# Performance work log

Hardware: AMD Instinct MI355X
Metric: run time of the kernel (lower is better)

Reference implementation:

```python
import jax, jax.numpy as jnp
import numpy as np

GRID_SIZE = 5
SPLINE_ORDER = 3


def _haar_filters():
    # db1 (Haar) decomposition filters, matching wavelet.create_wavelet_filter:
    # dec_lo[::-1] = [s, s], dec_hi[::-1] = [s, -s]; rec filters are identical for Haar.
    s = np.float32(1.0 / np.sqrt(2.0))
    lo = np.array([s, s], np.float32)
    hi = np.array([s, -s], np.float32)
    # f = a.unsqueeze(0) * b.unsqueeze(1)  ->  f[p, q] = a[q] * b[p]
    def outer(a, b):
        return b[:, None] * a[None, :]
    dec = np.stack([outer(lo, lo), outer(lo, hi), outer(hi, lo), outer(hi, hi)], 0)  # (4,2,2): LL,LH,HL,HH
    return jnp.asarray(dec), jnp.asarray(dec)


def depthwise_conv5(x, w, b):
    # torch Conv2d(C, C, 5, padding='same', groups=C)
    y = jax.lax.conv_general_dilated(
        x, w, window_strides=(1, 1), padding=[(2, 2), (2, 2)],
        dimension_numbers=('NCHW', 'OIHW', 'NCHW'), feature_group_count=x.shape[1])
    return y + b[None, :, None, None]


def kan_linear(x, base_w, spline_w, scaler):
    # efficient-kan KANLinear: base SiLU linear + B-spline linear over last dim.
    in_f = x.shape[-1]
    out_f = base_w.shape[0]
    shp = x.shape
    xf = x.reshape(-1, in_f)                      # (N, in)
    h = 2.0 / GRID_SIZE                           # grid_range [-1, 1]
    grid_1d = jnp.arange(-SPLINE_ORDER, GRID_SIZE + SPLINE_ORDER + 1, dtype=xf.dtype) * h - 1.0
    grid = jnp.broadcast_to(grid_1d, (in_f, grid_1d.shape[0]))  # (in, G+2k+1)
    xe = xf[:, :, None]
    bases = ((xe >= grid[:, :-1]) & (xe < grid[:, 1:])).astype(xf.dtype)
    for k in range(1, SPLINE_ORDER + 1):
        bases = ((xe - grid[:, :-(k + 1)]) / (grid[:, k:-1] - grid[:, :-(k + 1)]) * bases[..., :-1]
                 + (grid[:, k + 1:] - xe) / (grid[:, k + 1:] - grid[:, 1:-k]) * bases[..., 1:])
    # bases: (N, in, G+k)
    base_out = jax.nn.silu(xf) @ base_w.T
    sw = spline_w * scaler[:, :, None]            # scaled_spline_weight (out, in, G+k)
    spline_out = jnp.einsum('nig,oig->no', bases, sw)
    return (base_out + spline_out).reshape(*shp[:-1], out_f)


def setup_inputs() -> dict:
    key = jax.random.key(0)
    ks = jax.random.split(key, 6)
    C, H, W, B = 32, 256, 256, 4
    in_f = C * 4  # 128
    return {
        'x': jax.random.normal(ks[0], (B, C, H, W), jnp.float32),
        'conv_w': jax.random.normal(ks[1], (C, 1, 5, 5), jnp.float32) * 0.2,
        'conv_b': jax.random.normal(ks[2], (C,), jnp.float32) * 0.02,
        'kan_base_w': jax.random.normal(ks[3], (in_f, in_f), jnp.float32) * (1.0 / np.sqrt(in_f)),
        'kan_spline_w': jax.random.normal(ks[4], (in_f, in_f, GRID_SIZE + SPLINE_ORDER), jnp.float32) * 0.1,
        'kan_spline_scaler': 1.0 + 0.1 * jax.random.normal(ks[5], (in_f, in_f), jnp.float32),
    }


def reference(x, conv_w, conv_b, kan_base_w, kan_spline_w, kan_spline_scaler):
    dec, rec = _haar_filters()
    b, c, hh, ww = x.shape
    # Level-1 skip: depthwise base_conv on full-res input
    skip = depthwise_conv5(x, conv_w, conv_b)
    # Haar wavelet transform (stride-2 non-overlapping 2x2 depthwise conv) via reshape+einsum
    x5 = x.reshape(b, c, hh // 2, 2, ww // 2, 2)
    wt = jnp.einsum('bcipjq,kpq->bckij', x5, dec)  # (b, c, 4, h/2, w/2)
    # Subband KAN over last (width) dim of 128 == in_channels*4 -> msi_kan branch
    z = kan_linear(wt, kan_base_w, kan_spline_w, kan_spline_scaler)
    # Inverse wavelet (stride-2 conv_transpose) via einsum scatter
    y = jnp.einsum('bckij,kpq->bcipjq', z, rec).reshape(b, c, hh, ww)
    return y + skip
```

## Files before the change

### kernel.cpp

```cpp
#include <hip/hip_runtime.h>
#include <hip/hip_bf16.h>

using f32x4 = __attribute__((ext_vector_type(4))) float;
using s16x8 = __attribute__((ext_vector_type(8))) short;
using u32x4 = __attribute__((ext_vector_type(4))) unsigned;

constexpr int Bn = 4, Cc = 32, Hh = 256, Ww = 256;
constexpr int H2 = 128, W2 = 128;
constexpr int NF = 128;
constexpr int KTOT = 1152;

__device__ __forceinline__ short f2bf(float f) {
    union { float f; unsigned u; } v; v.f = f;
    unsigned r = v.u + 0x7fffu + ((v.u >> 16) & 1u);
    return (short)(r >> 16);
}

__device__ __forceinline__ unsigned pk_bf16(float a, float b) {
    union { __hip_bfloat162 h; unsigned u; } c;
    c.h.x = __float2bfloat16(a);
    c.h.y = __float2bfloat16(b);
    return c.u;
}

__device__ __forceinline__ void gload_lds16(const void* g, void* l) {
    __builtin_amdgcn_global_load_lds(
        (const __attribute__((address_space(1))) unsigned*)g,
        (__attribute__((address_space(3))) unsigned*)l, 16, 0, 0);
}

__device__ __forceinline__ void window128(float wD, float wC, float wB, float wA,
                                          int ci, unsigned W[4]) {
    unsigned long long P = ((unsigned long long)pk_bf16(wB, wA) << 32)
                         | (unsigned long long)pk_bf16(wD, wC);
    int sh = ci * 16 - 48;
    unsigned long long sl = P << (sh & 63);
    unsigned long long sr = P >> ((-sh) & 63);
    unsigned long long lo = (sh < 0) ? sr : ((sh < 64) ? sl : 0ull);
    int shh = sh - 64;
    unsigned long long sl2 = P << (shh & 63);
    unsigned long long sr2 = P >> ((-shh) & 63);
    unsigned long long hi = (shh >= 0) ? sl2 : (((-shh) < 64) ? sr2 : 0ull);
    W[0] = (unsigned)lo; W[1] = (unsigned)(lo >> 32);
    W[2] = (unsigned)hi; W[3] = (unsigned)(hi >> 32);
}

__global__ __launch_bounds__(256) void k_wbuild(const float* __restrict__ base_w,
                                                const float* __restrict__ spline_w,
                                                const float* __restrict__ scaler,
                                                short* __restrict__ Bg) {
    int idx = blockIdx.x * 256 + threadIdx.x;
    int tile = idx >> 9;
    int r = idx & 511;
    int lane = r >> 3, q = r & 7;
    int ni = tile / 36; int rem = tile - ni * 36;
    int jg = rem / 9;   int ks = rem - jg * 9;
    int o = ni * 16 + (lane & 15);
    int kk = ks * 32 + (lane >> 4) * 8 + q;
    int g = kk >> 5, jl = kk & 31;
    int j = jg * 32 + jl;
    float v = (g == 0) ? base_w[o * NF + j]
                       : spline_w[(long)(o * NF + j) * 8 + (g - 1)] * scaler[o * NF + j];
    Bg[idx] = f2bf(v);
}

__global__ __launch_bounds__(512, 4) void k_fused(const float* __restrict__ x,
                                                  const float* __restrict__ cw,
                                                  const float* __restrict__ cb,
                                                  float* __restrict__ out,
                                                  const short* __restrict__ Bg) {
    __shared__ __align__(16) short Bsh[72 * 512];
    const int t = threadIdx.x;
    const int lane = t & 63;
    const int wv = t >> 6;
    const int kcomp = wv & 3;
    const int mih = wv >> 2;
    const int blk = blockIdx.x;
    const int plane = blk >> 2;
    const int band = blk & 3;
    const int i0 = band << 5;
    const int jg0 = blk & 3;
    const int il = lane & 15;
    const int fg = lane >> 4;

    const float sB = (kcomp & 2) ? -1.f : 1.f;
    const float sC = (kcomp & 1) ? -1.f : 1.f;
    const float sD = sB * sC;

    const float* xbase = x + (long)plane * Hh * Ww;
    const float* xr0 = xbase + (long)(2 * (i0 + mih * 16 + il)) * Ww;
    const float* xr1 = xr0 + Ww;

    f32x4 acc[8];
#pragma unroll
    for (int ni = 0; ni < 8; ++ni)
        acc[ni] = (f32x4){0.f, 0.f, 0.f, 0.f};

    for (int j = 0; j < 4; ++j) {
        const int jg = (jg0 + j) & 3;
        const int cb2 = jg * 64 + fg * 16;

#pragma unroll
        for (int s = 0; s < 9; ++s) {
            int q = s * 8 + wv;
            int nl = q / 9, ks = q - nl * 9;
            gload_lds16(&Bg[(long)(((nl * 4 + jg) * 9 + ks) << 9) + lane * 8],
                        &Bsh[q << 9]);
        }

        u32x4 afr[9];
#pragma unroll
        for (int p = 0; p < 4; ++p) {
            f32x4 va = *(const f32x4*)(xr0 + cb2 + 4 * p);
            f32x4 vb = *(const f32x4*)(xr1 + cb2 + 4 * p);
            float vv[2];
            vv[0] = 0.5f * (va[0] + sB * va[1] + sC * vb[0] + sD * vb[1]);
            vv[1] = 0.5f * (va[2] + sB * va[3] + sC * vb[2] + sD * vb[3]);
            float sl2[2]; unsigned Wf[2][4];
#pragma unroll
            for (int e = 0; e < 2; ++e) {
                float v = vv[e];
                float ex = __builtin_amdgcn_exp2f(-1.442695040888963f * v);
                sl2[e] = v * __builtin_amdgcn_rcpf(1.0f + ex);
                float xs = __builtin_fmaf(v, 2.5f, 5.5f);
                xs = fminf(fmaxf(xs, 0.0f), 10.999f);
                float cf = floorf(xs);
                float u = xs - cf;
                int ci = (int)cf;
                float u2 = u * u, u3 = u2 * u;
                float wA = u3 * (1.f / 6.f);
                float wB = (1.f + 3.f * u + 3.f * u2 - 3.f * u3) * (1.f / 6.f);
                float wC = (4.f - 6.f * u2 + 3.f * u3) * (1.f / 6.f);
                float um = 1.f - u;
                float wD = um * um * um * (1.f / 6.f);
                window128(wD, wC, wB, wA, ci, Wf[e]);
            }
            afr[0][p] = pk_bf16(sl2[0], sl2[1]);
#pragma unroll
            for (int g = 1; g <= 8; ++g) {
                int wq = (g - 1) >> 1;
                unsigned sel = ((g - 1) & 1) ? 0x07060302u : 0x05040100u;
                afr[g][p] = __builtin_amdgcn_perm(Wf[1][wq], Wf[0][wq], sel);
            }
        }

        __syncthreads();

#pragma unroll
        for (int ks = 0; ks < 9; ++ks) {
            s16x8 bfr[8];
#pragma unroll
            for (int ni = 0; ni < 8; ++ni)
                bfr[ni] = *(const s16x8*)&Bsh[((ni * 9 + ks) << 9) + lane * 8];
            s16x8 a = __builtin_bit_cast(s16x8, afr[ks]);
#pragma unroll
            for (int ni = 0; ni < 8; ++ni)
                acc[ni] = __builtin_amdgcn_mfma_f32_16x16x32_bf16(
                    a, bfr[ni], acc[ni], 0, 0, 0);
        }
        __syncthreads();
    }

    constexpr int ZP = 132;
    float* zsh = (float*)Bsh;
#pragma unroll
    for (int rr = 0; rr < 4; ++rr)
#pragma unroll
        for (int ni = 0; ni < 8; ++ni)
            zsh[(kcomp * 32 + mih * 16 + fg * 4 + rr) * ZP + ni * 16 + il]
                = acc[ni][rr];
    __syncthreads();

    const int c = plane & 31;
    float cwr[25];
#pragma unroll
    for (int q = 0; q < 25; ++q) cwr[q] = cw[c * 25 + q];
    const float bias = cb[c];
    float* outp = out + (long)plane * Hh * Ww;

#pragma unroll
    for (int qxh = 0; qxh < 2; ++qxh) {
        const int jq = qxh * 64 + lane;
        const float mlo = (jq >= 1) ? 1.f : 0.f;
        const float mhi = (jq <= 126) ? 1.f : 0.f;
        const int clo = (jq >= 1) ? (2 * jq - 2) : 0;
        const int cmid = 2 * jq;
        const int chi = (jq <= 126) ? (2 * jq + 2) : 252;
        float xv[6][6];
#pragma unroll
        for (int a = 0; a < 4; ++a) {
            const int ql = wv * 4 + a;
            const int orow = 2 * (i0 + ql);
            const int rlo = (a == 0) ? 0 : 4;
            if (a) {
#pragma unroll
                for (int r6 = 0; r6 < 4; ++r6)
#pragma unroll
                    for (int c6 = 0; c6 < 6; ++c6) xv[r6][c6] = xv[r6 + 2][c6];
            }
#pragma unroll
            for (int r6 = 0; r6 < 6; ++r6) {
                if (r6 < rlo) continue;
                int xr = orow - 2 + r6;
                int xrc = min(max(xr, 0), Hh - 1);
                float mrow = (xr >= 0 && xr < Hh) ? 1.f : 0.f;
                const float* xrp = xbase + (long)xrc * Ww;
                float2 lo = *(const float2*)(xrp + clo);
                float2 mi2 = *(const float2*)(xrp + cmid);
                float2 hi = *(const float2*)(xrp + chi);
                float ml = mlo * mrow, mh = mhi * mrow;
                xv[r6][0] = lo.x * ml;    xv[r6][1] = lo.y * ml;
                xv[r6][2] = mi2.x * mrow; xv[r6][3] = mi2.y * mrow;
                xv[r6][4] = hi.x * mh;    xv[r6][5] = hi.y * mh;
            }
            float z0 = zsh[(ql) * ZP + jq];
            float z1 = zsh[(32 + ql) * ZP + jq];
            float z2 = zsh[(64 + ql) * ZP + jq];
            float z3 = zsh[(96 + ql) * ZP + jq];
            float y00 = 0.5f * (z0 + z1 + z2 + z3);
            float y01 = 0.5f * (z0 + z1 - z2 - z3);
            float y10 = 0.5f * (z0 - z1 + z2 - z3);
            float y11 = 0.5f * (z0 - z1 - z2 + z3);
            float s00 = bias, s01 = bias, s10 = bias, s11 = bias;
#pragma unroll
            for (int ky = 0; ky < 5; ++ky)
#pragma unroll
                for (int kx = 0; kx < 5; ++kx) {
                    float wv2 = cwr[ky * 5 + kx];
                    s00 += wv2 * xv[ky][kx];
                    s01 += wv2 * xv[ky][kx + 1];
                    s10 += wv2 * xv[ky + 1][kx];
                    s11 += wv2 * xv[ky + 1][kx + 1];
                }
            float* op = outp + (long)orow * Ww + 2 * jq;
            *(float2*)op        = make_float2(s00 + y00, s01 + y01);
            *(float2*)(op + Ww) = make_float2(s10 + y10, s11 + y11);
        }
    }
}

extern "C" void kernel_launch(void* const* d_in, const int* in_sizes, int n_in,
                              void* d_out, int out_size, void* d_ws, size_t ws_size,
                              hipStream_t stream) {
    const float* x        = (const float*)d_in[0];
    const float* conv_w   = (const float*)d_in[1];
    const float* conv_b   = (const float*)d_in[2];
    const float* base_w   = (const float*)d_in[3];
    const float* spline_w = (const float*)d_in[4];
    const float* scaler   = (const float*)d_in[5];
    float* out = (float*)d_out;
    short* Bg  = (short*)d_ws;

    k_wbuild<<<(NF * KTOT) / 256, 256, 0, stream>>>(base_w, spline_w, scaler, Bg);
    k_fused<<<512, 512, 0, stream>>>(x, conv_w, conv_b, out, Bg);
}
```

Baseline: 54.51 us.

## Double-buffer LDS weight tiles and overlap loads with MFMA compute

Splits each 72-tile weight stage into two 36-tile halves held in two LDS buffers. The next half is prefetched into the idle buffer while MFMAs run on the current one, and the A-fragment expansion for the next column group runs after the second half. The goal is to hide global-to-LDS load latency that used to stall before each compute phase, and the LDS footprint stays the same. The cost is twice as many barriers. Accumulators are also indexed by the loop parity, which could spill to scratch if the loop is not fully unrolled.

```diff
diff --git a/kernel.cpp b/kernel.cpp
--- a/kernel.cpp
+++ b/kernel.cpp
@@ -69,7 +69,7 @@
                                                   const float* __restrict__ cb,
                                                   float* __restrict__ out,
                                                   const short* __restrict__ Bg) {
-    __shared__ __align__(16) short Bsh[72 * 512];
+    __shared__ __align__(16) short Bsh[2][36 * 512];
     const int t = threadIdx.x;
     const int lane = t & 63;
     const int wv = t >> 6;
@@ -91,24 +91,10 @@
     const float* xr0 = xbase + (long)(2 * (i0 + mih * 16 + il)) * Ww;
     const float* xr1 = xr0 + Ww;
 
-    f32x4 acc[8];
-#pragma unroll
-    for (int ni = 0; ni < 8; ++ni)
-        acc[ni] = (f32x4){0.f, 0.f, 0.f, 0.f};
-
-    for (int j = 0; j < 4; ++j) {
-        const int jg = (jg0 + j) & 3;
+    u32x4 afr[9];
+
+    auto expansion = [&](int jg) {
         const int cb2 = jg * 64 + fg * 16;
-
-#pragma unroll
-        for (int s = 0; s < 9; ++s) {
-            int q = s * 8 + wv;
-            int nl = q / 9, ks = q - nl * 9;
-            gload_lds16(&Bg[(long)(((nl * 4 + jg) * 9 + ks) << 9) + lane * 8],
-                        &Bsh[q << 9]);
-        }
-
-        u32x4 afr[9];
 #pragma unroll
         for (int p = 0; p < 4; ++p) {
             f32x4 va = *(const f32x4*)(xr0 + cb2 + 4 * p);
@@ -143,24 +129,52 @@
                 afr[g][p] = __builtin_amdgcn_perm(Wf[1][wq], Wf[0][wq], sel);
             }
         }
-
+    };
+
+    auto stage_issue = [&](int jg, int nh, int buf) {
+#pragma unroll
+        for (int i = 0; i < 5; ++i) {
+            int q = i * 8 + wv;
+            if (q < 36) {
+                int nl = q / 9, ks = q - nl * 9;
+                int ng = nh * 4 + nl;
+                gload_lds16(&Bg[(long)(((ng * 4 + jg) * 9 + ks) << 9) + lane * 8],
+                            &Bsh[buf][q << 9]);
+            }
+        }
+    };
+
+    f32x4 acc[8];
+#pragma unroll
+    for (int ni = 0; ni < 8; ++ni)
+        acc[ni] = (f32x4){0.f, 0.f, 0.f, 0.f};
+
+    stage_issue(jg0, 0, 0);
+    expansion(jg0);
+
+    for (int s = 0; s < 8; ++s) {
+        const int nh = s & 1;
         __syncthreads();
-
+        if (s < 7) {
+            const int s1 = s + 1;
+            stage_issue((jg0 + (s1 >> 1)) & 3, s1 & 1, s1 & 1);
+        }
 #pragma unroll
         for (int ks = 0; ks < 9; ++ks) {
-            s16x8 bfr[8];
-#pragma unroll
-            for (int ni = 0; ni < 8; ++ni)
-                bfr[ni] = *(const s16x8*)&Bsh[((ni * 9 + ks) << 9) + lane * 8];
+            s16x8 bfr[4];
+#pragma unroll
+            for (int nl = 0; nl < 4; ++nl)
+                bfr[nl] = *(const s16x8*)&Bsh[s & 1][((nl * 9 + ks) << 9) + lane * 8];
             s16x8 a = __builtin_bit_cast(s16x8, afr[ks]);
 #pragma unroll
-            for (int ni = 0; ni < 8; ++ni)
-                acc[ni] = __builtin_amdgcn_mfma_f32_16x16x32_bf16(
-                    a, bfr[ni], acc[ni], 0, 0, 0);
-        }
-        __syncthreads();
+            for (int nl = 0; nl < 4; ++nl)
+                acc[nh * 4 + nl] = __builtin_amdgcn_mfma_f32_16x16x32_bf16(
+                    a, bfr[nl], acc[nh * 4 + nl], 0, 0, 0);
+        }
+        if ((s & 1) && s < 7) expansion((jg0 + (s >> 1) + 1) & 3);
     }
 
+    __syncthreads();
     constexpr int ZP = 132;
     float* zsh = (float*)Bsh;
 #pragma unroll
```

Result: slower. 81.57 us (+49.6%).
